# Optimization experiments

Hardware: AMD Instinct MI355X
Metric: run time of the kernel (lower is better)

Reference implementation:

```python
import jax, jax.numpy as jnp
from jax import lax
import numpy as np

IN, HID, NCLS, B, S = 360, 64, 5, 64, 128
MH_CONST = 2.0 / (np.sqrt(3.0) * np.pi ** 0.25)


def setup_inputs() -> dict:
    key = jax.random.key(0)
    ks = jax.random.split(key, 24)
    g = lambda i, shape, s=0.05: jax.random.normal(ks[i], shape, jnp.float32) * s
    inp = {
        'x_seq': jax.random.normal(ks[0], (B, S, IN), jnp.float32),
        # WavKANLinear params (out=64, in=360)
        'wav_scale': jnp.ones((HID, IN), jnp.float32),
        'wav_translation': jnp.zeros((HID, IN), jnp.float32),
        'wav_weights': g(1, (HID, IN)),
        'base_weight': g(2, (HID, IN)),
        # BatchNorm1d (eval mode, running stats)
        'bn_gamma': jnp.ones((HID,), jnp.float32),
        'bn_beta': jnp.zeros((HID,), jnp.float32),
        'bn_mean': jnp.zeros((HID,), jnp.float32),
        'bn_var': jnp.ones((HID,), jnp.float32),
        # LayerNorm(64)
        'ln_gamma': jnp.ones((HID,), jnp.float32),
        'ln_beta': jnp.zeros((HID,), jnp.float32),
        # bidirectional GRU, 1 layer, hidden=64
        'gru_w_ih_f': g(3, (3 * HID, HID)), 'gru_w_hh_f': g(4, (3 * HID, HID)),
        'gru_b_ih_f': g(5, (3 * HID,)), 'gru_b_hh_f': g(6, (3 * HID,)),
        'gru_w_ih_b': g(7, (3 * HID, HID)), 'gru_w_hh_b': g(8, (3 * HID, HID)),
        'gru_b_ih_b': g(9, (3 * HID,)), 'gru_b_hh_b': g(10, (3 * HID,)),
        # classifier: Linear(128,64) -> ReLU -> Linear(64,5)
        'fc1_w': g(11, (HID, 2 * HID)), 'fc1_b': jnp.zeros((HID,), jnp.float32),
        'fc2_w': g(12, (NCLS, HID)), 'fc2_b': jnp.zeros((NCLS,), jnp.float32),
    }
    return inp


def _gru_dir(x_sbf, w_ih, w_hh, b_ih, b_hh, reverse):
    # x_sbf: (S, B, F). Returns final hidden (B, H). PyTorch GRU equations.
    Bn = x_sbf.shape[1]
    H = w_hh.shape[1]
    gi_all = jnp.einsum('sbf,gf->sbg', x_sbf, w_ih) + b_ih  # precompute input gates

    def step(h, gi):
        gh = h @ w_hh.T + b_hh
        i_r, i_z, i_n = jnp.split(gi, 3, axis=-1)
        h_r, h_z, h_n = jnp.split(gh, 3, axis=-1)
        r = jax.nn.sigmoid(i_r + h_r)
        z = jax.nn.sigmoid(i_z + h_z)
        n = jnp.tanh(i_n + r * h_n)
        h_new = (1.0 - z) * n + z * h
        return h_new, None

    h0 = jnp.zeros((Bn, H), x_sbf.dtype)
    h_final, _ = lax.scan(step, h0, gi_all, reverse=reverse)
    return h_final


def reference(x_seq, wav_scale, wav_translation, wav_weights, base_weight,
              bn_gamma, bn_beta, bn_mean, bn_var, ln_gamma, ln_beta,
              gru_w_ih_f, gru_w_hh_f, gru_b_ih_f, gru_b_hh_f,
              gru_w_ih_b, gru_w_hh_b, gru_b_ih_b, gru_b_hh_b,
              fc1_w, fc1_b, fc2_w, fc2_b):
    b, s, f = x_seq.shape
    x_flat = x_seq.reshape(b * s, f)  # (N, 360)

    # --- WavKANLinear (mexican_hat) ---
    x_scaled = (x_flat[:, None, :] - wav_translation[None]) / wav_scale[None]  # (N, 64, 360)
    wavelet = MH_CONST * (x_scaled * x_scaled - 1.0) * jnp.exp(-0.5 * x_scaled * x_scaled)
    wav_out = jnp.einsum('noi,oi->no', wavelet, wav_weights)  # (N, 64)
    base_out = jax.nn.silu(x_flat) @ base_weight.T
    combined = wav_out + base_out
    # BatchNorm1d eval mode
    x_emb = (combined - bn_mean) * lax.rsqrt(bn_var + 1e-5) * bn_gamma + bn_beta

    # --- LayerNorm(64) ---
    mu = jnp.mean(x_emb, axis=-1, keepdims=True)
    var = jnp.mean(jnp.square(x_emb - mu), axis=-1, keepdims=True)
    x_emb = (x_emb - mu) * lax.rsqrt(var + 1e-5) * ln_gamma + ln_beta
    # dropout is identity in eval mode

    x_sbf = x_emb.reshape(b, s, HID).swapaxes(0, 1)  # (S, B, 64)

    # --- bidirectional GRU, take final hiddens ---
    h_fwd = _gru_dir(x_sbf, gru_w_ih_f, gru_w_hh_f, gru_b_ih_f, gru_b_hh_f, False)
    h_bwd = _gru_dir(x_sbf, gru_w_ih_b, gru_w_hh_b, gru_b_ih_b, gru_b_hh_b, True)
    hidden_cat = jnp.concatenate([h_fwd, h_bwd], axis=1)  # (B, 128)

    # --- classifier ---
    h = jax.nn.relu(hidden_cat @ fc1_w.T + fc1_b)
    logits = h @ fc2_w.T + fc2_b
    return logits
```

## Files before the change

kernel.cpp:

```cpp
#include <hip/hip_runtime.h>

#define IN_F   360
#define HIDN   64
#define NCLS   5
#define BATCH  64
#define SEQ    128
#define NROWS  (BATCH*SEQ)

#define WS_FLAG  0
#define WS_WPACK 16
#define WS_WFAST 92176
#define WS_WT4   138256
#define WS_XEMB  162832
#define WS_GI    687120
#define WS_HC    3832848

#define LOG2E        1.4426950408889634f
#define NEG_HALF_L2E (-0.7213475204444817f)

__device__ __forceinline__ float fast_rcp(float x) { return __builtin_amdgcn_rcpf(x); }
__device__ __forceinline__ float fast_rsq(float x) { return __builtin_amdgcn_rsqf(x); }
__device__ __forceinline__ float sigmoid_(float x) {
    x = fminf(fmaxf(x, -60.0f), 60.0f);
    return fast_rcp(1.0f + exp2f(-LOG2E * x));
}
__device__ __forceinline__ float tanh_(float x) {
    x = fminf(fmaxf(x, -30.0f), 30.0f);
    float e = exp2f(-2.8853900817779268f * x);
    return (1.0f - e) * fast_rcp(1.0f + e);
}

__global__ __launch_bounds__(256) void prep_kernel(
    const float* __restrict__ scale, const float* __restrict__ trans,
    const float* __restrict__ ww,    const float* __restrict__ bw,
    const float* __restrict__ wihf,  const float* __restrict__ wihb,
    float* __restrict__ ws) {
    int idx = blockIdx.x * 256 + threadIdx.x;
    float4* wpack  = (float4*)(ws + WS_WPACK);
    float2* wfast2 = (float2*)(ws + WS_WFAST);
    float*  wT4    = ws + WS_WT4;
    int*    flagp  = (int*)(ws + WS_FLAG);
    if (idx < 64 * IN_F) {
        int o = idx & 63, i = idx >> 6;
        float s  = scale[o * IN_F + i];
        float tr = trans[o * IN_F + i];
        if (s != 1.0f || tr != 0.0f) atomicOr(flagp, 1);
        float a  = 1.0f / s;
        float b  = -tr * a;
        float wq = 0.8673250705840776f * ww[o * IN_F + i];
        float bb = bw[o * IN_F + i];
        wpack[i * 64 + o] = make_float4(a, b, wq, bb);
        wfast2[(i >> 1) * 128 + o * 2 + (i & 1)] = make_float2(wq, bb);
    }
    int idx2 = idx - 64 * IN_F;
    if (idx2 >= 0 && idx2 < 24576) {
        int e = idx2 & 3; int rest = idx2 >> 2;
        int g = rest % 384; int k4 = rest / 384;
        int k = k4 * 4 + e; int dir = g / 192; int gg = g - dir * 192;
        const float* src = dir ? wihb : wihf;
        wT4[idx2] = src[gg * 64 + k];
    }
}

__global__ __launch_bounds__(256) void wavkan_kernel(
    const float* __restrict__ x_seq,
    const float* __restrict__ bn_g, const float* __restrict__ bn_b,
    const float* __restrict__ bn_m, const float* __restrict__ bn_v,
    const float* __restrict__ ln_g, const float* __restrict__ ln_b,
    const float* __restrict__ ws_c, float* __restrict__ x_emb) {
    __shared__ float2 xs_lds[16 * IN_F];
    int t = threadIdx.x;
    int row0 = blockIdx.x * 16;
    int o = t & 63, grp = t >> 6;
    int fast = (*(const int*)(ws_c + WS_FLAG)) == 0;

    float acc0 = 0.f, acc1 = 0.f, acc2 = 0.f, acc3 = 0.f;

    if (fast) {
        for (int idx = t; idx < 16 * IN_F; idx += 256) {
            int r = idx / IN_F, i = idx - r * IN_F;
            float x = x_seq[(row0 + r) * IN_F + i];
            float u = x * x;
            float phi = (u - 1.0f) * exp2f(u * NEG_HALF_L2E);
            float sl  = x * fast_rcp(1.0f + exp2f(-LOG2E * x));
            xs_lds[idx] = make_float2(phi, sl);
        }
        __syncthreads();
        const float4* wf4 = (const float4*)(ws_c + WS_WFAST);
        const float4* xs4 = (const float4*)xs_lds;
        const float4* xr0 = xs4 + (grp * 4 + 0) * 180;
        const float4* xr1 = xs4 + (grp * 4 + 1) * 180;
        const float4* xr2 = xs4 + (grp * 4 + 2) * 180;
        const float4* xr3 = xs4 + (grp * 4 + 3) * 180;
        #pragma unroll 2
        for (int i2 = 0; i2 < 180; ++i2) {
            float4 wp = wf4[i2 * 64 + o];
            float4 a = xr0[i2];
            acc0 = fmaf(a.x, wp.x, acc0); acc0 = fmaf(a.y, wp.y, acc0);
            acc0 = fmaf(a.z, wp.z, acc0); acc0 = fmaf(a.w, wp.w, acc0);
            float4 b = xr1[i2];
            acc1 = fmaf(b.x, wp.x, acc1); acc1 = fmaf(b.y, wp.y, acc1);
            acc1 = fmaf(b.z, wp.z, acc1); acc1 = fmaf(b.w, wp.w, acc1);
            float4 c = xr2[i2];
            acc2 = fmaf(c.x, wp.x, acc2); acc2 = fmaf(c.y, wp.y, acc2);
            acc2 = fmaf(c.z, wp.z, acc2); acc2 = fmaf(c.w, wp.w, acc2);
            float4 d = xr3[i2];
            acc3 = fmaf(d.x, wp.x, acc3); acc3 = fmaf(d.y, wp.y, acc3);
            acc3 = fmaf(d.z, wp.z, acc3); acc3 = fmaf(d.w, wp.w, acc3);
        }
    } else {
        for (int idx = t; idx < 16 * IN_F; idx += 256) {
            int r = idx / IN_F, i = idx - r * IN_F;
            float x = x_seq[(row0 + r) * IN_F + i];
            float sl = x * fast_rcp(1.0f + exp2f(-LOG2E * x));
            xs_lds[idx] = make_float2(x, sl);
        }
        __syncthreads();
        const float4* wpack = (const float4*)(ws_c + WS_WPACK);
        const float2* xr0 = xs_lds + (grp * 4 + 0) * IN_F;
        const float2* xr1 = xs_lds + (grp * 4 + 1) * IN_F;
        const float2* xr2 = xs_lds + (grp * 4 + 2) * IN_F;
        const float2* xr3 = xs_lds + (grp * 4 + 3) * IN_F;
        for (int i = 0; i < IN_F; ++i) {
            float4 wp = wpack[i * 64 + o];
            {
                float2 xs = xr0[i];
                float xsc = fmaf(xs.x, wp.x, wp.y); float u = xsc * xsc;
                float e = exp2f(u * NEG_HALF_L2E);
                acc0 = fmaf((u - 1.0f) * e, wp.z, acc0);
                acc0 = fmaf(xs.y, wp.w, acc0);
            }
            {
                float2 xs = xr1[i];
                float xsc = fmaf(xs.x, wp.x, wp.y); float u = xsc * xsc;
                float e = exp2f(u * NEG_HALF_L2E);
                acc1 = fmaf((u - 1.0f) * e, wp.z, acc1);
                acc1 = fmaf(xs.y, wp.w, acc1);
            }
            {
                float2 xs = xr2[i];
                float xsc = fmaf(xs.x, wp.x, wp.y); float u = xsc * xsc;
                float e = exp2f(u * NEG_HALF_L2E);
                acc2 = fmaf((u - 1.0f) * e, wp.z, acc2);
                acc2 = fmaf(xs.y, wp.w, acc2);
            }
            {
                float2 xs = xr3[i];
                float xsc = fmaf(xs.x, wp.x, wp.y); float u = xsc * xsc;
                float e = exp2f(u * NEG_HALF_L2E);
                acc3 = fmaf((u - 1.0f) * e, wp.z, acc3);
                acc3 = fmaf(xs.y, wp.w, acc3);
            }
        }
    }

    float bscale = bn_g[o] * fast_rsq(bn_v[o] + 1e-5f);
    float bshift = fmaf(-bn_m[o], bscale, bn_b[o]);
    float lg = ln_g[o], lb = ln_b[o];
    float vals[4] = {acc0, acc1, acc2, acc3};
    #pragma unroll
    for (int rr = 0; rr < 4; ++rr) {
        float y = fmaf(vals[rr], bscale, bshift);
        float s = y;
        #pragma unroll
        for (int m = 1; m < 64; m <<= 1) s += __shfl_xor(s, m, 64);
        float mu = s * (1.0f / 64.0f);
        float d = y - mu;
        float s2 = d * d;
        #pragma unroll
        for (int m = 1; m < 64; m <<= 1) s2 += __shfl_xor(s2, m, 64);
        float rstd = fast_rsq(s2 * (1.0f / 64.0f) + 1e-5f);
        x_emb[(row0 + grp * 4 + rr) * 64 + o] = fmaf(d * rstd, lg, lb);
    }
}

__global__ __launch_bounds__(384) void gi_kernel(
    const float* __restrict__ ws_c,
    const float* __restrict__ bihf, const float* __restrict__ bihb,
    float* __restrict__ gi) {
    const float4* wT4   = (const float4*)(ws_c + WS_WT4);
    const float*  x_emb = ws_c + WS_XEMB;
    int g = threadIdx.x;
    int dir = g / 192, gg = g - dir * 192;
    float bih = dir ? bihb[gg] : bihf[gg];
    float4 w[16];
    #pragma unroll
    for (int k4 = 0; k4 < 16; ++k4) w[k4] = wT4[k4 * 384 + g];
    int n0 = blockIdx.x * 16;
    for (int rr = 0; rr < 16; ++rr) {
        int n = n0 + rr;
        const float4* xr = (const float4*)(x_emb + n * 64);
        float acc = bih;
        #pragma unroll
        for (int k4 = 0; k4 < 16; ++k4) {
            float4 xv = xr[k4]; float4 wv = w[k4];
            acc = fmaf(xv.x, wv.x, acc); acc = fmaf(xv.y, wv.y, acc);
            acc = fmaf(xv.z, wv.z, acc); acc = fmaf(xv.w, wv.w, acc);
        }
        gi[n * 384 + g] = acc;
    }
}

__global__ __launch_bounds__(192) void gru_kernel(
    const float* __restrict__ ws_c,
    const float* __restrict__ whhf, const float* __restrict__ bhhf,
    const float* __restrict__ whhb, const float* __restrict__ bhhb,
    float* __restrict__ hc) {
    __shared__ __align__(16) float h_lds[3][64];
    __shared__ float gh[2][192];
    const float* gi = ws_c + WS_GI;
    int t = threadIdx.x, wave = t >> 6, lane = t & 63;
    int b = blockIdx.x & 63, dir = blockIdx.x >> 6;
    const float* whh = dir ? whhb : whhf;
    const float* bhh = dir ? bhhb : bhhf;
    float4 w[16];
    const float4* wrow = (const float4*)(whh + t * 64);
    #pragma unroll
    for (int q = 0; q < 16; ++q) w[q] = wrow[q];
    float bias = bhh[t];
    h_lds[wave][lane] = 0.0f;
    float hreg = 0.0f;

    int s0 = dir ? (SEQ - 1) : 0;
    int base0 = (b * SEQ + s0) * 384 + dir * 192;
    float ir  = gi[base0 + lane];
    float iz  = gi[base0 + 64 + lane];
    float in_ = gi[base0 + 128 + lane];
    __syncthreads();

    for (int ss = 0; ss < SEQ; ++ss) {
        float nir = 0.f, niz = 0.f, nin = 0.f;
        if (ss < SEQ - 1) {
            int s2 = dir ? (SEQ - 2 - ss) : (ss + 1);
            int base = (b * SEQ + s2) * 384 + dir * 192;
            nir = gi[base + lane];
            niz = gi[base + 64 + lane];
            nin = gi[base + 128 + lane];
        }
        const float4* h4 = (const float4*)h_lds[wave];
        float a0 = 0.f, a1 = 0.f, a2 = 0.f, a3 = 0.f;
        #pragma unroll
        for (int q = 0; q < 16; ++q) {
            float4 hv = h4[q]; float4 wv = w[q];
            a0 = fmaf(hv.x, wv.x, a0); a1 = fmaf(hv.y, wv.y, a1);
            a2 = fmaf(hv.z, wv.z, a2); a3 = fmaf(hv.w, wv.w, a3);
        }
        int p = ss & 1;
        gh[p][t] = bias + ((a0 + a1) + (a2 + a3));
        __syncthreads();
        float ghr = gh[p][lane], ghz = gh[p][64 + lane], ghn = gh[p][128 + lane];
        float r = sigmoid_(ir + ghr);
        float z = sigmoid_(iz + ghz);
        float n = tanh_(fmaf(r, ghn, in_));
        hreg = fmaf(z, hreg - n, n);
        h_lds[wave][lane] = hreg;
        ir = nir; iz = niz; in_ = nin;
    }
    if (t < 64) hc[b * 128 + dir * 64 + lane] = hreg;
}

__global__ __launch_bounds__(64) void head_kernel(
    const float* __restrict__ ws_c,
    const float* __restrict__ fc1w, const float* __restrict__ fc1b,
    const float* __restrict__ fc2w, const float* __restrict__ fc2b,
    float* __restrict__ out) {
    __shared__ __align__(16) float hr[128];
    __shared__ float h1[64];
    const float* hc = ws_c + WS_HC;
    int bb = blockIdx.x, t = threadIdx.x;
    hr[t]      = hc[bb * 128 + t];
    hr[64 + t] = hc[bb * 128 + 64 + t];
    __syncthreads();
    float acc = fc1b[t];
    const float4* w4 = (const float4*)(fc1w + t * 128);
    const float4* h4 = (const float4*)hr;
    #pragma unroll 8
    for (int k4 = 0; k4 < 32; ++k4) {
        float4 wv = w4[k4]; float4 hv = h4[k4];
        acc = fmaf(hv.x, wv.x, acc); acc = fmaf(hv.y, wv.y, acc);
        acc = fmaf(hv.z, wv.z, acc); acc = fmaf(hv.w, wv.w, acc);
    }
    h1[t] = fmaxf(acc, 0.0f);
    __syncthreads();
    if (t < NCLS) {
        float acc2 = fc2b[t];
        const float* wr = fc2w + t * 64;
        #pragma unroll 8
        for (int k = 0; k < 64; ++k) acc2 = fmaf(h1[k], wr[k], acc2);
        out[bb * NCLS + t] = acc2;
    }
}

extern "C" void kernel_launch(void* const* d_in, const int* in_sizes, int n_in,
                              void* d_out, int out_size, void* d_ws, size_t ws_size,
                              hipStream_t stream) {
    const float* x_seq = (const float*)d_in[0];
    const float* wscal = (const float*)d_in[1];
    const float* wtran = (const float*)d_in[2];
    const float* wwght = (const float*)d_in[3];
    const float* bwght = (const float*)d_in[4];
    const float* bn_g  = (const float*)d_in[5];
    const float* bn_b  = (const float*)d_in[6];
    const float* bn_m  = (const float*)d_in[7];
    const float* bn_v  = (const float*)d_in[8];
    const float* ln_g  = (const float*)d_in[9];
    const float* ln_b  = (const float*)d_in[10];
    const float* wihf  = (const float*)d_in[11];
    const float* whhf  = (const float*)d_in[12];
    const float* bihf  = (const float*)d_in[13];
    const float* bhhf  = (const float*)d_in[14];
    const float* wihb  = (const float*)d_in[15];
    const float* whhb  = (const float*)d_in[16];
    const float* bihb  = (const float*)d_in[17];
    const float* bhhb  = (const float*)d_in[18];
    const float* fc1w  = (const float*)d_in[19];
    const float* fc1b  = (const float*)d_in[20];
    const float* fc2w  = (const float*)d_in[21];
    const float* fc2b  = (const float*)d_in[22];
    float* ws  = (float*)d_ws;
    float* out = (float*)d_out;

    hipMemsetAsync(ws + WS_FLAG, 0, sizeof(int), stream);
    hipLaunchKernelGGL(prep_kernel, dim3(186), dim3(256), 0, stream,
                       wscal, wtran, wwght, bwght, wihf, wihb, ws);
    hipLaunchKernelGGL(wavkan_kernel, dim3(NROWS / 16), dim3(256), 0, stream,
                       x_seq, bn_g, bn_b, bn_m, bn_v, ln_g, ln_b, ws, ws + WS_XEMB);
    hipLaunchKernelGGL(gi_kernel, dim3(NROWS / 16), dim3(384), 0, stream,
                       ws, bihf, bihb, ws + WS_GI);
    hipLaunchKernelGGL(gru_kernel, dim3(128), dim3(192), 0, stream,
                       ws, whhf, bhhf, whhb, bhhb, ws + WS_HC);
    hipLaunchKernelGGL(head_kernel, dim3(64), dim3(64), 0, stream,
                       ws, fc1w, fc1b, fc2w, fc2b, out);
}
```

Before: 257.2 us.

## Run GRU recurrence in a single wave with shuffles and stage gi inputs in LDS

The GRU recurrence moves from three waves that exchange gate sums through LDS with a __syncthreads every step to one 64-lane wave. Each lane holds all three gate weight rows (192 registers) and broadcasts h with __shfl, so the per-step block barrier goes away and the input-gate loads are prefetched two steps ahead. The gi projection now stages 32 x_emb rows in LDS and computes two rows at a time. The risks are heavy register pressure, and the serial step now issues three times as many FMAs and 64 shuffles in a single wave.

After: 297.4 us. 1.16x slower.

```diff
diff --git a/kernel.cpp b/kernel.cpp
--- a/kernel.cpp
+++ b/kernel.cpp
@@ -178,85 +178,110 @@
     const float* __restrict__ ws_c,
     const float* __restrict__ bihf, const float* __restrict__ bihb,
     float* __restrict__ gi) {
+    __shared__ __align__(16) float xs[32 * 64];
     const float4* wT4   = (const float4*)(ws_c + WS_WT4);
     const float*  x_emb = ws_c + WS_XEMB;
-    int g = threadIdx.x;
-    int dir = g / 192, gg = g - dir * 192;
+    int t = threadIdx.x;
+    int row0 = blockIdx.x * 32;
+    {
+        const float4* src = (const float4*)(x_emb + row0 * 64);
+        float4* dst = (float4*)xs;
+        for (int i = t; i < 512; i += 384) dst[i] = src[i];
+    }
+    int dir = t / 192, gg = t - dir * 192;
     float bih = dir ? bihb[gg] : bihf[gg];
     float4 w[16];
     #pragma unroll
-    for (int k4 = 0; k4 < 16; ++k4) w[k4] = wT4[k4 * 384 + g];
-    int n0 = blockIdx.x * 16;
-    for (int rr = 0; rr < 16; ++rr) {
-        int n = n0 + rr;
-        const float4* xr = (const float4*)(x_emb + n * 64);
-        float acc = bih;
-        #pragma unroll
-        for (int k4 = 0; k4 < 16; ++k4) {
-            float4 xv = xr[k4]; float4 wv = w[k4];
-            acc = fmaf(xv.x, wv.x, acc); acc = fmaf(xv.y, wv.y, acc);
-            acc = fmaf(xv.z, wv.z, acc); acc = fmaf(xv.w, wv.w, acc);
-        }
-        gi[n * 384 + g] = acc;
-    }
-}
-
-__global__ __launch_bounds__(192) void gru_kernel(
+    for (int k4 = 0; k4 < 16; ++k4) w[k4] = wT4[k4 * 384 + t];
+    __syncthreads();
+    for (int r = 0; r < 32; r += 2) {
+        const float4* x0 = (const float4*)(xs + r * 64);
+        const float4* x1 = (const float4*)(xs + r * 64 + 64);
+        float a0 = bih, a1 = 0.f, b0 = bih, b1 = 0.f;
+        #pragma unroll
+        for (int k4 = 0; k4 < 16; k4 += 2) {
+            float4 xv = x0[k4];     float4 wv = w[k4];
+            a0 = fmaf(xv.x, wv.x, a0); a0 = fmaf(xv.y, wv.y, a0);
+            a0 = fmaf(xv.z, wv.z, a0); a0 = fmaf(xv.w, wv.w, a0);
+            float4 xu = x0[k4 + 1]; float4 wu = w[k4 + 1];
+            a1 = fmaf(xu.x, wu.x, a1); a1 = fmaf(xu.y, wu.y, a1);
+            a1 = fmaf(xu.z, wu.z, a1); a1 = fmaf(xu.w, wu.w, a1);
+            float4 yv = x1[k4];
+            b0 = fmaf(yv.x, wv.x, b0); b0 = fmaf(yv.y, wv.y, b0);
+            b0 = fmaf(yv.z, wv.z, b0); b0 = fmaf(yv.w, wv.w, b0);
+            float4 yu = x1[k4 + 1];
+            b1 = fmaf(yu.x, wu.x, b1); b1 = fmaf(yu.y, wu.y, b1);
+            b1 = fmaf(yu.z, wu.z, b1); b1 = fmaf(yu.w, wu.w, b1);
+        }
+        gi[(row0 + r) * 384 + t]     = a0 + a1;
+        gi[(row0 + r + 1) * 384 + t] = b0 + b1;
+    }
+}
+
+__global__ __launch_bounds__(64, 1) void gru_kernel(
     const float* __restrict__ ws_c,
     const float* __restrict__ whhf, const float* __restrict__ bhhf,
     const float* __restrict__ whhb, const float* __restrict__ bhhb,
     float* __restrict__ hc) {
-    __shared__ __align__(16) float h_lds[3][64];
-    __shared__ float gh[2][192];
     const float* gi = ws_c + WS_GI;
-    int t = threadIdx.x, wave = t >> 6, lane = t & 63;
+    int lane = threadIdx.x;
     int b = blockIdx.x & 63, dir = blockIdx.x >> 6;
     const float* whh = dir ? whhb : whhf;
     const float* bhh = dir ? bhhb : bhhf;
-    float4 w[16];
-    const float4* wrow = (const float4*)(whh + t * 64);
-    #pragma unroll
-    for (int q = 0; q < 16; ++q) w[q] = wrow[q];
-    float bias = bhh[t];
-    h_lds[wave][lane] = 0.0f;
+
+    float wr[64], wz[64], wn[64];
+    {
+        const float4* pr = (const float4*)(whh + lane * 64);
+        const float4* pz = (const float4*)(whh + (64 + lane) * 64);
+        const float4* pn = (const float4*)(whh + (128 + lane) * 64);
+        #pragma unroll
+        for (int q = 0; q < 16; ++q) {
+            float4 a = pr[q];
+            wr[4*q] = a.x; wr[4*q+1] = a.y; wr[4*q+2] = a.z; wr[4*q+3] = a.w;
+            float4 c = pz[q];
+            wz[4*q] = c.x; wz[4*q+1] = c.y; wz[4*q+2] = c.z; wz[4*q+3] = c.w;
+            float4 d = pn[q];
+            wn[4*q] = d.x; wn[4*q+1] = d.y; wn[4*q+2] = d.z; wn[4*q+3] = d.w;
+        }
+    }
+    float br = bhh[lane], bz = bhh[64 + lane], bnn = bhh[128 + lane];
     float hreg = 0.0f;
-
+    int step = dir ? -1 : 1;
     int s0 = dir ? (SEQ - 1) : 0;
-    int base0 = (b * SEQ + s0) * 384 + dir * 192;
-    float ir  = gi[base0 + lane];
-    float iz  = gi[base0 + 64 + lane];
-    float in_ = gi[base0 + 128 + lane];
-    __syncthreads();
+    const float* gbase = gi + (b * SEQ) * 384 + dir * 192 + lane;
+
+    float ir  = gbase[s0 * 384],          iz  = gbase[s0 * 384 + 64],          inn = gbase[s0 * 384 + 128];
+    float ir1 = gbase[(s0 + step) * 384], iz1 = gbase[(s0 + step) * 384 + 64], in1 = gbase[(s0 + step) * 384 + 128];
 
     for (int ss = 0; ss < SEQ; ++ss) {
         float nir = 0.f, niz = 0.f, nin = 0.f;
-        if (ss < SEQ - 1) {
-            int s2 = dir ? (SEQ - 2 - ss) : (ss + 1);
-            int base = (b * SEQ + s2) * 384 + dir * 192;
-            nir = gi[base + lane];
-            niz = gi[base + 64 + lane];
-            nin = gi[base + 128 + lane];
-        }
-        const float4* h4 = (const float4*)h_lds[wave];
-        float a0 = 0.f, a1 = 0.f, a2 = 0.f, a3 = 0.f;
-        #pragma unroll
-        for (int q = 0; q < 16; ++q) {
-            float4 hv = h4[q]; float4 wv = w[q];
-            a0 = fmaf(hv.x, wv.x, a0); a1 = fmaf(hv.y, wv.y, a1);
-            a2 = fmaf(hv.z, wv.z, a2); a3 = fmaf(hv.w, wv.w, a3);
-        }
-        int p = ss & 1;
-        gh[p][t] = bias + ((a0 + a1) + (a2 + a3));
-        __syncthreads();
-        float ghr = gh[p][lane], ghz = gh[p][64 + lane], ghn = gh[p][128 + lane];
-        float r = sigmoid_(ir + ghr);
-        float z = sigmoid_(iz + ghz);
-        float n = tanh_(fmaf(r, ghn, in_));
+        if (ss < SEQ - 2) {
+            int ai = (s0 + (ss + 2) * step) * 384;
+            nir = gbase[ai]; niz = gbase[ai + 64]; nin = gbase[ai + 128];
+        }
+        float ar0 = ir + br, ar1 = 0.f, ar2 = 0.f, ar3 = 0.f;
+        float az0 = iz + bz, az1 = 0.f, az2 = 0.f, az3 = 0.f;
+        float an0 = bnn,     an1 = 0.f, an2 = 0.f, an3 = 0.f;
+        #pragma unroll
+        for (int k = 0; k < 64; k += 4) {
+            float h0 = __shfl(hreg, k, 64);
+            float h1 = __shfl(hreg, k + 1, 64);
+            float h2 = __shfl(hreg, k + 2, 64);
+            float h3 = __shfl(hreg, k + 3, 64);
+            ar0 = fmaf(wr[k],     h0, ar0); az0 = fmaf(wz[k],     h0, az0); an0 = fmaf(wn[k],     h0, an0);
+            ar1 = fmaf(wr[k + 1], h1, ar1); az1 = fmaf(wz[k + 1], h1, az1); an1 = fmaf(wn[k + 1], h1, an1);
+            ar2 = fmaf(wr[k + 2], h2, ar2); az2 = fmaf(wz[k + 2], h2, az2); an2 = fmaf(wn[k + 2], h2, an2);
+            ar3 = fmaf(wr[k + 3], h3, ar3); az3 = fmaf(wz[k + 3], h3, az3); an3 = fmaf(wn[k + 3], h3, an3);
+        }
+        float r = sigmoid_((ar0 + ar1) + (ar2 + ar3));
+        float z = sigmoid_((az0 + az1) + (az2 + az3));
+        float ghn = (an0 + an1) + (an2 + an3);
+        float n = tanh_(fmaf(r, ghn, inn));
         hreg = fmaf(z, hreg - n, n);
-        h_lds[wave][lane] = hreg;
-        ir = nir; iz = niz; in_ = nin;
-    }
-    if (t < 64) hc[b * 128 + dir * 64 + lane] = hreg;
+        ir = ir1; iz = iz1; inn = in1;
+        ir1 = nir; iz1 = niz; in1 = nin;
+    }
+    hc[b * 128 + dir * 64 + lane] = hreg;
 }
 
 __global__ __launch_bounds__(64) void head_kernel(
@@ -325,9 +350,9 @@
                        wscal, wtran, wwght, bwght, wihf, wihb, ws);
     hipLaunchKernelGGL(wavkan_kernel, dim3(NROWS / 16), dim3(256), 0, stream,
                        x_seq, bn_g, bn_b, bn_m, bn_v, ln_g, ln_b, ws, ws + WS_XEMB);
-    hipLaunchKernelGGL(gi_kernel, dim3(NROWS / 16), dim3(384), 0, stream,
+    hipLaunchKernelGGL(gi_kernel, dim3(NROWS / 32), dim3(384), 0, stream,
                        ws, bihf, bihb, ws + WS_GI);
-    hipLaunchKernelGGL(gru_kernel, dim3(128), dim3(192), 0, stream,
+    hipLaunchKernelGGL(gru_kernel, dim3(128), dim3(64), 0, stream,
                        ws, whhf, bhhf, whhb, bhhb, ws + WS_HC);
     hipLaunchKernelGGL(head_kernel, dim3(64), dim3(64), 0, stream,
                        ws, fc1w, fc1b, fc2w, fc2b, out);
```
